# Performance work log

Measured on AMD Instinct MI355X. Metric: run time of the kernel, lower is better.

Reference implementation:

```python
import jax, jax.numpy as jnp
from jax import lax
import numpy as np

NUM_LAYERS, HIDDEN, INPUT, OUT = 6, 256, 128, 10
B, T = 128, 512


def setup_inputs() -> dict:
    key = jax.random.key(0)
    ks = jax.random.split(key, 9)
    s = 0.05  # keep gate pre-activations in a sane range
    return {
        "x": jax.random.normal(ks[0], (B, T, INPUT), jnp.float32),
        "h0": jax.random.normal(ks[1], (NUM_LAYERS, B, HIDDEN), jnp.float32) * s,
        "c0": jax.random.normal(ks[2], (NUM_LAYERS, B, HIDDEN), jnp.float32) * s,
        "w_ih": jax.random.normal(ks[3], (NUM_LAYERS, 4 * HIDDEN, HIDDEN), jnp.float32) * s,
        "w_hh": jax.random.normal(ks[4], (NUM_LAYERS, 4 * HIDDEN, HIDDEN), jnp.float32) * s,
        "b_ih": jax.random.normal(ks[5], (NUM_LAYERS, 4 * HIDDEN), jnp.float32) * s,
        "b_hh": jax.random.normal(ks[6], (NUM_LAYERS, 4 * HIDDEN), jnp.float32) * s,
        "fc_w": jax.random.normal(ks[7], (OUT, HIDDEN), jnp.float32) * s,
        "fc_b": jax.random.normal(ks[8], (OUT,), jnp.float32) * s,
    }


def _lstm_layer(xseq, h, c, wih, whh, bih, bhh):
    # xseq: [B,T,D]; precompute input-to-gate GEMM for the whole sequence.
    gx = jnp.einsum("btd,gd->btg", xseq, wih) + (bih + bhh)  # [B,T,4H]

    def step(carry, g_t):
        h, c = carry
        g = g_t + h @ whh.T  # [B,4H], PyTorch gate order i,f,g,o
        i, f, gg, o = jnp.split(g, 4, axis=-1)
        c = jax.nn.sigmoid(f) * c + jax.nn.sigmoid(i) * jnp.tanh(gg)
        h = jax.nn.sigmoid(o) * jnp.tanh(c)
        return (h, c), h

    (_, _), hs = lax.scan(step, (h, c), jnp.swapaxes(gx, 0, 1))  # hs: [T,B,H]
    return jnp.swapaxes(hs, 0, 1)  # [B,T,H]


def reference(x, h0, c0, w_ih, w_hh, b_ih, b_hh, fc_w, fc_b):
    # Zero-pad input features 128 -> 256 so the packed [4H,256] layer-0 w_ih
    # applies identically to using its first 128 columns.
    seq = jnp.pad(x, ((0, 0), (0, 0), (0, HIDDEN - INPUT)))
    for l in range(NUM_LAYERS):
        seq = _lstm_layer(seq, h0[l], c0[l], w_ih[l], w_hh[l], b_ih[l], b_hh[l])
    return seq[:, -1, :] @ fc_w.T + fc_b  # [B,OUT]
```

## Files before the change

### kernel.cpp

```cpp
#include <hip/hip_runtime.h>
#include <stdint.h>

#define NLAYER 6
#define BATCH  128
#define HID    256
#define TSEQ   512
#define INFEAT 128
#define DEPTH  8
#define OUTN   10

typedef __attribute__((ext_vector_type(8))) short bf16x8;
typedef __attribute__((ext_vector_type(4))) float f32x4;

__device__ __forceinline__ short f2bf(float f) {
  union { float f; uint32_t u; } v; v.f = f;
  uint32_t r = v.u + 0x7fffu + ((v.u >> 16) & 1u);
  return (short)(r >> 16);
}
__device__ __forceinline__ float bf2f(uint32_t b) {
  union { uint32_t u; float f; } v; v.u = b << 16;
  return v.f;
}
__device__ __forceinline__ bf16x8 cvt8(const float* p) {
  f32x4 a = *(const f32x4*)p;
  f32x4 b = *(const f32x4*)(p + 4);
  bf16x8 r;
  r[0] = f2bf(a[0]); r[1] = f2bf(a[1]); r[2] = f2bf(a[2]); r[3] = f2bf(a[3]);
  r[4] = f2bf(b[0]); r[5] = f2bf(b[1]); r[6] = f2bf(b[2]); r[7] = f2bf(b[3]);
  return r;
}
__device__ __forceinline__ float sigm(float x)  { return 1.0f / (1.0f + __expf(-x)); }
__device__ __forceinline__ float tanhff(float x){ return 1.0f - 2.0f / (__expf(2.0f * x) + 1.0f); }

__device__ __forceinline__ bf16x8 load_frag_dc(const uint16_t* p) {
  union { unsigned long long q[2]; bf16x8 v; } u;
  u.q[0] = __hip_atomic_load((const unsigned long long*)p,
                             __ATOMIC_RELAXED, __HIP_MEMORY_SCOPE_AGENT);
  u.q[1] = __hip_atomic_load((const unsigned long long*)(p + 4),
                             __ATOMIC_RELAXED, __HIP_MEMORY_SCOPE_AGENT);
  return u.v;
}
__device__ __forceinline__ void store_u16_dc(uint16_t* p, uint16_t v) {
  __hip_atomic_store(p, v, __ATOMIC_RELAXED, __HIP_MEMORY_SCOPE_AGENT);
}
__device__ __forceinline__ void store_u8_dc(uint8_t* p, uint8_t v) {
  __hip_atomic_store(p, v, __ATOMIC_RELAXED, __HIP_MEMORY_SCOPE_AGENT);
}
__device__ __forceinline__ bool rec_half(const uint8_t* f) {
  unsigned long long a = __hip_atomic_load((const unsigned long long*)f,
                                           __ATOMIC_RELAXED, __HIP_MEMORY_SCOPE_AGENT);
  unsigned long long b = __hip_atomic_load((const unsigned long long*)(f + 8),
                                           __ATOMIC_RELAXED, __HIP_MEMORY_SCOPE_AGENT);
  return ((a & b) == 0x0101010101010101ULL);
}

__global__ void __launch_bounds__(256, 1)
lstm_pipeline(const float* __restrict__ xin, const float* __restrict__ h0,
              const float* __restrict__ c0,  const float* __restrict__ wih,
              const float* __restrict__ whh, const float* __restrict__ bih,
              const float* __restrict__ bhh, const float* __restrict__ fcw,
              const float* __restrict__ fcb, float* __restrict__ out,
              uint8_t* flags, uint16_t* hbuf)
{
  const int bid  = blockIdx.x;
  const int xcd  = bid & 7;
  const int slot = bid >> 3;
  const int grp  = (slot >> 3) * 8 + xcd;
  const int cg   = slot & 7;
  const int l  = grp >> 2;
  const int bs = grp & 3;

  const int tid  = threadIdx.x;
  const int wv   = tid >> 6, lane = tid & 63;
  const int wm   = wv & 1,  wu   = wv >> 1;
  const int l15  = lane & 15, l4 = lane >> 4;

  __shared__ bf16x8 lds_wih[4096];
  {
    const float* W = wih + (size_t)l * 1024 * 256;
    for (int lin = tid; lin < 4096; lin += 256) {
      const int l4s = lin & 3;
      const int u5  = (lin >> 2) & 31;
      const int kk  = (lin >> 7) & 7;
      const int gt  = lin >> 10;
      const int row = gt * 256 + cg * 32 + u5;
      lds_wih[lin] = cvt8(W + (size_t)row * 256 + kk * 32 + l4s * 8);
    }
  }

  bf16x8 wh[4][8];
  float  bias[4];
  {
    const float* W = whh + (size_t)l * 1024 * 256;
#pragma unroll
    for (int gt = 0; gt < 4; ++gt) {
      const int Rg = gt * 256 + cg * 32 + wu * 16 + l15;
      const float* rp = W + (size_t)Rg * 256 + l4 * 8;
#pragma unroll
      for (int kk = 0; kk < 8; ++kk)
        wh[gt][kk] = cvt8(rp + kk * 32);
      bias[gt] = bih[l * 1024 + Rg] + bhh[l * 1024 + Rg];
    }
  }
  __syncthreads();

  const int ucol  = cg * 32 + wu * 16 + l15;
  const int mrowA = bs * 32 + wm * 16 + l15;
  const int mrow0 = bs * 32 + wm * 16 + l4*4;

  float c[4];
#pragma unroll
  for (int j = 0; j < 4; ++j)
    c[j] = c0[((size_t)l * BATCH + (mrow0 + j)) * HID + ucol];

  const uint8_t* fXr = (l > 0) ? flags + ((size_t)((l - 1) * 4 + bs) * TSEQ) * 32 : nullptr;
  uint8_t*       fOr = flags + ((size_t)grp * TSEQ) * 32;
  const uint8_t* fCr = (l < 5) ? flags + ((size_t)((l + 1) * 4 + bs) * TSEQ) * 32 : nullptr;

  const uint16_t* hbL = hbuf + (size_t)l * DEPTH * BATCH * HID;
  const uint16_t* hbX = (l > 0) ? hbuf + (size_t)(l - 1) * DEPTH * BATCH * HID : nullptr;
  uint16_t*       hbO = hbuf + (size_t)l * DEPTH * BATCH * HID;

  const int fidx = wm * 16 + cg * 2 + wu;

  for (int t = 0; t < TSEQ; ++t) {
    {
      bool needx = (l > 0), needh = (t > 0);
      const uint8_t* fx = needx ? fXr + (size_t)t * 32 + wm * 16 : nullptr;
      const uint8_t* fo = needh ? fOr + (size_t)(t - 1) * 32 + wm * 16 : nullptr;
      while (needx || needh) {
        if (needx && rec_half(fx)) needx = false;
        if (needh && rec_half(fo)) needh = false;
      }
    }

    bf16x8 ah[8];
    if (t == 0) {
      const float* hp = h0 + ((size_t)l * BATCH + mrowA) * HID + l4 * 8;
#pragma unroll
      for (int kk = 0; kk < 8; ++kk) ah[kk] = cvt8(hp + kk * 32);
    } else {
      const uint16_t* hp = hbL + ((size_t)((t - 1) & (DEPTH - 1)) * BATCH + mrowA) * HID + l4 * 8;
#pragma unroll
      for (int kk = 0; kk < 8; ++kk) ah[kk] = load_frag_dc(hp + kk * 32);
    }

    f32x4 acc[4];
#pragma unroll
    for (int gt = 0; gt < 4; ++gt) {
      f32x4 a = {bias[gt], bias[gt], bias[gt], bias[gt]};
      acc[gt] = a;
    }

    const int bbase = (wu * 16 + l15) * 4 + l4;
    if (l == 0) {
      const float* xp = xin + ((size_t)mrowA * TSEQ + t) * INFEAT + l4 * 8;
#pragma unroll
      for (int kk = 0; kk < 4; ++kk) {
        bf16x8 axr = cvt8(xp + kk * 32);
#pragma unroll
        for (int gt = 0; gt < 4; ++gt) {
          bf16x8 b = lds_wih[gt * 1024 + kk * 128 + bbase];
          acc[gt] = __builtin_amdgcn_mfma_f32_16x16x32_bf16(axr, b, acc[gt], 0, 0, 0);
        }
      }
    } else {
      bf16x8 ax[8];
      const uint16_t* hp = hbX + ((size_t)(t & (DEPTH - 1)) * BATCH + mrowA) * HID + l4 * 8;
#pragma unroll
      for (int kk = 0; kk < 8; ++kk) ax[kk] = load_frag_dc(hp + kk * 32);
#pragma unroll
      for (int kk = 0; kk < 8; ++kk) {
#pragma unroll
        for (int gt = 0; gt < 4; ++gt) {
          bf16x8 b = lds_wih[gt * 1024 + kk * 128 + bbase];
          acc[gt] = __builtin_amdgcn_mfma_f32_16x16x32_bf16(ax[kk], b, acc[gt], 0, 0, 0);
        }
      }
    }

#pragma unroll
    for (int kk = 0; kk < 8; ++kk)
#pragma unroll
      for (int gt = 0; gt < 4; ++gt)
        acc[gt] = __builtin_amdgcn_mfma_f32_16x16x32_bf16(ah[kk], wh[gt][kk], acc[gt], 0, 0, 0);

    if (l < 5 && t >= DEPTH) {
      const uint8_t* fc = fCr + (size_t)(t - DEPTH) * 32 + wm * 16;
      while (!rec_half(fc)) __builtin_amdgcn_s_sleep(2);
    }

    uint16_t* op = hbO + (size_t)(t & (DEPTH - 1)) * BATCH * HID;
#pragma unroll
    for (int j = 0; j < 4; ++j) {
      float iv = sigm(acc[0][j]);
      float fv = sigm(acc[1][j]);
      float gv = tanhff(acc[2][j]);
      float ov = sigm(acc[3][j]);
      float cc = fv * c[j] + iv * gv;
      c[j] = cc;
      float hv = ov * tanhff(cc);
      store_u16_dc(op + (size_t)(mrow0 + j) * HID + ucol, (uint16_t)f2bf(hv));
    }
    asm volatile("s_waitcnt vmcnt(0)" ::: "memory");
    if (lane == 0)
      store_u8_dc(fOr + (size_t)t * 32 + fidx, (uint8_t)1);
  }

  if (l == 5 && cg == 0) {
    const uint8_t* fl = fOr + (size_t)(TSEQ - 1) * 32;
    while (!(rec_half(fl) && rec_half(fl + 16))) __builtin_amdgcn_s_sleep(1);
    const uint16_t* hp = hbL + (size_t)((TSEQ - 1) & (DEPTH - 1)) * BATCH * HID;
    for (int p = tid; p < 32 * OUTN; p += 256) {
      const int mr = bs * 32 + p / OUTN, oc = p % OUTN;
      float a = fcb[oc];
      const uint16_t* hr = hp + (size_t)mr * HID;
      const float* wr = fcw + oc * HID;
#pragma unroll
      for (int uu = 0; uu < HID; uu += 4) {
        unsigned long long q = __hip_atomic_load((const unsigned long long*)(hr + uu),
                                                 __ATOMIC_RELAXED, __HIP_MEMORY_SCOPE_AGENT);
        a += bf2f((uint32_t)(q & 0xffff))         * wr[uu]
           + bf2f((uint32_t)((q >> 16) & 0xffff)) * wr[uu + 1]
           + bf2f((uint32_t)((q >> 32) & 0xffff)) * wr[uu + 2]
           + bf2f((uint32_t)(q >> 48))            * wr[uu + 3];
      }
      out[mr * OUTN + oc] = a;
    }
  }
}

extern "C" void kernel_launch(void* const* d_in, const int* in_sizes, int n_in,
                              void* d_out, int out_size, void* d_ws, size_t ws_size,
                              hipStream_t stream) {
  const float* xin = (const float*)d_in[0];
  const float* h0  = (const float*)d_in[1];
  const float* c0  = (const float*)d_in[2];
  const float* wih = (const float*)d_in[3];
  const float* whh = (const float*)d_in[4];
  const float* bih = (const float*)d_in[5];
  const float* bhh = (const float*)d_in[6];
  const float* fcw = (const float*)d_in[7];
  const float* fcb = (const float*)d_in[8];
  float* out = (float*)d_out;

  uint8_t* flags = (uint8_t*)d_ws;
  const size_t flagBytes = (size_t)24 * TSEQ * 32;
  uint16_t* hbuf = (uint16_t*)((char*)d_ws + 0x80000);

  hipMemsetAsync(d_ws, 0, flagBytes, stream);
  lstm_pipeline<<<dim3(192), dim3(256), 0, stream>>>(
      xin, h0, c0, wih, whh, bih, bhh, fcw, fcb, out, flags, hbuf);
}
```

Measured before the change: 3.419 ms.

## Replace per-step flag handshakes with tagged data words and progress counters

Each hidden-state store now packs two bf16 values with a 16-bit timestep tag into one 64-bit word. Consumers spin directly on the data until every tag matches, which removes the separate flag store and the vmcnt(0) drain that sat on the recurrent critical path. Back-pressure now uses per-wave progress counters instead of per-timestep flag arrays, the ring shrinks to depth 4, and the LDS weight layout is reordered. In exchange, ring traffic doubles because of the tag bits, and correctness relies on stale tags from earlier runs never matching, since the ring is no longer cleared.

```diff
diff --git a/kernel.cpp b/kernel.cpp
--- a/kernel.cpp
+++ b/kernel.cpp
@@ -6,11 +6,12 @@
 #define HID    256
 #define TSEQ   512
 #define INFEAT 128
-#define DEPTH  8
+#define DEPTH  4
 #define OUTN   10
 
 typedef __attribute__((ext_vector_type(8))) short bf16x8;
 typedef __attribute__((ext_vector_type(4))) float f32x4;
+typedef unsigned long long u64;
 
 __device__ __forceinline__ short f2bf(float f) {
   union { float f; uint32_t u; } v; v.f = f;
@@ -32,27 +33,16 @@
 __device__ __forceinline__ float sigm(float x)  { return 1.0f / (1.0f + __expf(-x)); }
 __device__ __forceinline__ float tanhff(float x){ return 1.0f - 2.0f / (__expf(2.0f * x) + 1.0f); }
 
-__device__ __forceinline__ bf16x8 load_frag_dc(const uint16_t* p) {
-  union { unsigned long long q[2]; bf16x8 v; } u;
-  u.q[0] = __hip_atomic_load((const unsigned long long*)p,
-                             __ATOMIC_RELAXED, __HIP_MEMORY_SCOPE_AGENT);
-  u.q[1] = __hip_atomic_load((const unsigned long long*)(p + 4),
-                             __ATOMIC_RELAXED, __HIP_MEMORY_SCOPE_AGENT);
-  return u.v;
-}
-__device__ __forceinline__ void store_u16_dc(uint16_t* p, uint16_t v) {
+__device__ __forceinline__ u64 ld64(const u64* p) {
+  return __hip_atomic_load(p, __ATOMIC_RELAXED, __HIP_MEMORY_SCOPE_AGENT);
+}
+__device__ __forceinline__ void st64(u64* p, u64 v) {
   __hip_atomic_store(p, v, __ATOMIC_RELAXED, __HIP_MEMORY_SCOPE_AGENT);
 }
-__device__ __forceinline__ void store_u8_dc(uint8_t* p, uint8_t v) {
+__device__ __forceinline__ void st16(uint16_t* p, uint16_t v) {
   __hip_atomic_store(p, v, __ATOMIC_RELAXED, __HIP_MEMORY_SCOPE_AGENT);
 }
-__device__ __forceinline__ bool rec_half(const uint8_t* f) {
-  unsigned long long a = __hip_atomic_load((const unsigned long long*)f,
-                                           __ATOMIC_RELAXED, __HIP_MEMORY_SCOPE_AGENT);
-  unsigned long long b = __hip_atomic_load((const unsigned long long*)(f + 8),
-                                           __ATOMIC_RELAXED, __HIP_MEMORY_SCOPE_AGENT);
-  return ((a & b) == 0x0101010101010101ULL);
-}
+
 
 __global__ void __launch_bounds__(256, 1)
 lstm_pipeline(const float* __restrict__ xin, const float* __restrict__ h0,
@@ -60,7 +50,7 @@
               const float* __restrict__ whh, const float* __restrict__ bih,
               const float* __restrict__ bhh, const float* __restrict__ fcw,
               const float* __restrict__ fcb, float* __restrict__ out,
-              uint8_t* flags, uint16_t* hbuf)
+              uint16_t* prog, u64* ring)
 {
   const int bid  = blockIdx.x;
   const int xcd  = bid & 7;
@@ -79,8 +69,8 @@
   {
     const float* W = wih + (size_t)l * 1024 * 256;
     for (int lin = tid; lin < 4096; lin += 256) {
-      const int l4s = lin & 3;
-      const int u5  = (lin >> 2) & 31;
+      const int u5  = lin & 31;
+      const int l4s = (lin >> 5) & 3;
       const int kk  = (lin >> 7) & 7;
       const int gt  = lin >> 10;
       const int row = gt * 256 + cg * 32 + u5;
@@ -106,43 +96,47 @@
 
   const int ucol  = cg * 32 + wu * 16 + l15;
   const int mrowA = bs * 32 + wm * 16 + l15;
-  const int mrow0 = bs * 32 + wm * 16 + l4*4;
+  const int mrow0 = bs * 32 + wm * 16 + l4 * 4;
 
   float c[4];
 #pragma unroll
   for (int j = 0; j < 4; ++j)
     c[j] = c0[((size_t)l * BATCH + (mrow0 + j)) * HID + ucol];
 
-  const uint8_t* fXr = (l > 0) ? flags + ((size_t)((l - 1) * 4 + bs) * TSEQ) * 32 : nullptr;
-  uint8_t*       fOr = flags + ((size_t)grp * TSEQ) * 32;
-  const uint8_t* fCr = (l < 5) ? flags + ((size_t)((l + 1) * 4 + bs) * TSEQ) * 32 : nullptr;
-
-  const uint16_t* hbL = hbuf + (size_t)l * DEPTH * BATCH * HID;
-  const uint16_t* hbX = (l > 0) ? hbuf + (size_t)(l - 1) * DEPTH * BATCH * HID : nullptr;
-  uint16_t*       hbO = hbuf + (size_t)l * DEPTH * BATCH * HID;
-
-  const int fidx = wm * 16 + cg * 2 + wu;
+  u64*       ringO = ring + (size_t)l * DEPTH * BATCH * 128;
+  const u64* ringL = ringO;
+  const u64* ringX = (l > 0) ? ring + (size_t)(l - 1) * DEPTH * BATCH * 128 : nullptr;
+
+  uint16_t* progOwn = prog + (l * 4 + bs) * 32;
+  const u64* progCons = (l < 5) ? (const u64*)(prog + ((l + 1) * 4 + bs) * 32) : nullptr;
+
+  const int srow = bs * 32 + wm * 16 + 15;
 
   for (int t = 0; t < TSEQ; ++t) {
+    if (lane == 0)
+      st16(progOwn + (cg * 4 + wv), (uint16_t)t);
+
     {
-      bool needx = (l > 0), needh = (t > 0);
-      const uint8_t* fx = needx ? fXr + (size_t)t * 32 + wm * 16 : nullptr;
-      const uint8_t* fo = needh ? fOr + (size_t)(t - 1) * 32 + wm * 16 : nullptr;
-      while (needx || needh) {
-        if (needx && rec_half(fx)) needx = false;
-        if (needh && rec_half(fo)) needh = false;
-      }
-    }
-
-    bf16x8 ah[8];
-    if (t == 0) {
-      const float* hp = h0 + ((size_t)l * BATCH + mrowA) * HID + l4 * 8;
-#pragma unroll
-      for (int kk = 0; kk < 8; ++kk) ah[kk] = cvt8(hp + kk * 32);
-    } else {
-      const uint16_t* hp = hbL + ((size_t)((t - 1) & (DEPTH - 1)) * BATCH + mrowA) * HID + l4 * 8;
-#pragma unroll
-      for (int kk = 0; kk < 8; ++kk) ah[kk] = load_frag_dc(hp + kk * 32);
+      const bool isH = (lane < 16), isX = (lane >= 16 && lane < 32);
+      const bool needS = (isH && t > 0) || (isX && l > 0);
+      const u64* sp = ringL;
+      u64 stag = 0;
+      if (isH && t > 0) {
+        const int cgp = lane >> 1, wup = lane & 1;
+        sp = ringL + (((size_t)((t - 1) & (DEPTH - 1)) * BATCH + srow) * 128 + cgp * 16 + wup * 8 + 7);
+        stag = (u64)t;
+      } else if (isX && l > 0) {
+        const int i = lane - 16, cgp = i >> 1, wup = i & 1;
+        sp = ringX + (((size_t)(t & (DEPTH - 1)) * BATCH + srow) * 128 + cgp * 16 + wup * 8 + 7);
+        stag = (u64)(t + 1);
+      }
+      if (t > 0 || l > 0) {
+        for (;;) {
+          int ok = 1;
+          if (needS) ok = ((ld64(sp) >> 48) == stag);
+          if (__all(ok)) break;
+        }
+      }
     }
 
     f32x4 acc[4];
@@ -152,45 +146,97 @@
       acc[gt] = a;
     }
 
-    const int bbase = (wu * 16 + l15) * 4 + l4;
+    const int bcol = wu * 16 + l15;
     if (l == 0) {
       const float* xp = xin + ((size_t)mrowA * TSEQ + t) * INFEAT + l4 * 8;
 #pragma unroll
       for (int kk = 0; kk < 4; ++kk) {
         bf16x8 axr = cvt8(xp + kk * 32);
 #pragma unroll
-        for (int gt = 0; gt < 4; ++gt) {
-          bf16x8 b = lds_wih[gt * 1024 + kk * 128 + bbase];
-          acc[gt] = __builtin_amdgcn_mfma_f32_16x16x32_bf16(axr, b, acc[gt], 0, 0, 0);
+        for (int gt = 0; gt < 4; ++gt)
+          acc[gt] = __builtin_amdgcn_mfma_f32_16x16x32_bf16(
+              axr, lds_wih[((gt * 8 + kk) * 4 + l4) * 32 + bcol], acc[gt], 0, 0, 0);
+      }
+    } else {
+      const u64* xb = ringX + ((size_t)(t & (DEPTH - 1)) * BATCH + mrowA) * 128 + l4 * 4;
+      const u64 tagX = (u64)(t + 1);
+      bf16x8 ax[8];
+      for (;;) {
+        u64 bad = 0;
+#pragma unroll
+        for (int kk = 0; kk < 8; ++kk) {
+          union { uint32_t w[4]; bf16x8 v; } u;
+#pragma unroll
+          for (int j = 0; j < 4; ++j) {
+            u64 r = ld64(xb + kk * 16 + j);
+            bad |= (r >> 48) ^ tagX;
+            u.w[j] = (uint32_t)r;
+          }
+          ax[kk] = u.v;
         }
+        if (__all(bad == 0)) break;
+      }
+#pragma unroll
+      for (int kk = 0; kk < 8; ++kk)
+#pragma unroll
+        for (int gt = 0; gt < 4; ++gt)
+          acc[gt] = __builtin_amdgcn_mfma_f32_16x16x32_bf16(
+              ax[kk], lds_wih[((gt * 8 + kk) * 4 + l4) * 32 + bcol], acc[gt], 0, 0, 0);
+    }
+
+    if (t == 0) {
+      const float* hp = h0 + ((size_t)l * BATCH + mrowA) * HID + l4 * 8;
+#pragma unroll
+      for (int kk = 0; kk < 8; ++kk) {
+        bf16x8 af = cvt8(hp + kk * 32);
+#pragma unroll
+        for (int gt = 0; gt < 4; ++gt)
+          acc[gt] = __builtin_amdgcn_mfma_f32_16x16x32_bf16(af, wh[gt][kk], acc[gt], 0, 0, 0);
       }
     } else {
-      bf16x8 ax[8];
-      const uint16_t* hp = hbX + ((size_t)(t & (DEPTH - 1)) * BATCH + mrowA) * HID + l4 * 8;
-#pragma unroll
-      for (int kk = 0; kk < 8; ++kk) ax[kk] = load_frag_dc(hp + kk * 32);
-#pragma unroll
-      for (int kk = 0; kk < 8; ++kk) {
-#pragma unroll
-        for (int gt = 0; gt < 4; ++gt) {
-          bf16x8 b = lds_wih[gt * 1024 + kk * 128 + bbase];
-          acc[gt] = __builtin_amdgcn_mfma_f32_16x16x32_bf16(ax[kk], b, acc[gt], 0, 0, 0);
+      const u64* hb = ringL + ((size_t)((t - 1) & (DEPTH - 1)) * BATCH + mrowA) * 128 + l4 * 4;
+      const u64 tagH = (u64)t;
+      bf16x8 ah[8];
+      for (;;) {
+        u64 bad = 0;
+#pragma unroll
+        for (int kk = 0; kk < 8; ++kk) {
+          union { uint32_t w[4]; bf16x8 v; } u;
+#pragma unroll
+          for (int j = 0; j < 4; ++j) {
+            u64 r = ld64(hb + kk * 16 + j);
+            bad |= (r >> 48) ^ tagH;
+            u.w[j] = (uint32_t)r;
+          }
+          ah[kk] = u.v;
         }
-      }
-    }
-
-#pragma unroll
-    for (int kk = 0; kk < 8; ++kk)
-#pragma unroll
-      for (int gt = 0; gt < 4; ++gt)
-        acc[gt] = __builtin_amdgcn_mfma_f32_16x16x32_bf16(ah[kk], wh[gt][kk], acc[gt], 0, 0, 0);
+        if (__all(bad == 0)) break;
+      }
+#pragma unroll
+      for (int kk = 0; kk < 8; ++kk)
+#pragma unroll
+        for (int gt = 0; gt < 4; ++gt)
+          acc[gt] = __builtin_amdgcn_mfma_f32_16x16x32_bf16(ah[kk], wh[gt][kk], acc[gt], 0, 0, 0);
+    }
 
     if (l < 5 && t >= DEPTH) {
-      const uint8_t* fc = fCr + (size_t)(t - DEPTH) * 32 + wm * 16;
-      while (!rec_half(fc)) __builtin_amdgcn_s_sleep(2);
-    }
-
-    uint16_t* op = hbO + (size_t)(t & (DEPTH - 1)) * BATCH * HID;
+      const int need = t - (DEPTH - 1);
+      for (;;) {
+        int mn = 0x7fffffff;
+#pragma unroll
+        for (int q = 0; q < 8; ++q) {
+          u64 v = ld64(progCons + q);
+          mn = min(mn, (int)(v & 0xffff));
+          mn = min(mn, (int)((v >> 16) & 0xffff));
+          mn = min(mn, (int)((v >> 32) & 0xffff));
+          mn = min(mn, (int)((v >> 48) & 0xffff));
+        }
+        if (mn >= need) break;
+        __builtin_amdgcn_s_sleep(2);
+      }
+    }
+
+    uint32_t hv16[4];
 #pragma unroll
     for (int j = 0; j < 4; ++j) {
       float iv = sigm(acc[0][j]);
@@ -200,30 +246,43 @@
       float cc = fv * c[j] + iv * gv;
       c[j] = cc;
       float hv = ov * tanhff(cc);
-      store_u16_dc(op + (size_t)(mrow0 + j) * HID + ucol, (uint16_t)f2bf(hv));
-    }
-    asm volatile("s_waitcnt vmcnt(0)" ::: "memory");
-    if (lane == 0)
-      store_u8_dc(fOr + (size_t)t * 32 + fidx, (uint8_t)1);
+      hv16[j] = (uint32_t)(uint16_t)f2bf(hv);
+    }
+    {
+      const uint32_t own01 = hv16[0] | (hv16[1] << 16);
+      const uint32_t own23 = hv16[2] | (hv16[3] << 16);
+      const uint32_t par01 = (uint32_t)__shfl_xor((int)own01, 1);
+      const uint32_t par23 = (uint32_t)__shfl_xor((int)own23, 1);
+      const u64 tagS = (u64)(t + 1) << 48;
+      uint32_t d0, d1; int j0;
+      if ((l15 & 1) == 0) {
+        d0 = (own01 & 0xffffu) | (par01 << 16);
+        d1 = (own01 >> 16)     | (par01 & 0xffff0000u);
+        j0 = 0;
+      } else {
+        d0 = (par23 & 0xffffu) | (own23 << 16);
+        d1 = (par23 >> 16)     | (own23 & 0xffff0000u);
+        j0 = 2;
+      }
+      u64* rp = ringO + ((size_t)(t & (DEPTH - 1)) * BATCH + (mrow0 + j0)) * 128 + (ucol >> 1);
+      st64(rp,       (u64)d0 | tagS);
+      st64(rp + 128, (u64)d1 | tagS);
+    }
   }
 
   if (l == 5 && cg == 0) {
-    const uint8_t* fl = fOr + (size_t)(TSEQ - 1) * 32;
-    while (!(rec_half(fl) && rec_half(fl + 16))) __builtin_amdgcn_s_sleep(1);
-    const uint16_t* hp = hbL + (size_t)((TSEQ - 1) & (DEPTH - 1)) * BATCH * HID;
+    const u64* hsl = ring + (size_t)5 * DEPTH * BATCH * 128
+                   + ((size_t)((TSEQ - 1) & (DEPTH - 1)) * BATCH) * 128;
     for (int p = tid; p < 32 * OUTN; p += 256) {
       const int mr = bs * 32 + p / OUTN, oc = p % OUTN;
       float a = fcb[oc];
-      const uint16_t* hr = hp + (size_t)mr * HID;
+      const u64* hr = hsl + (size_t)mr * 128;
       const float* wr = fcw + oc * HID;
-#pragma unroll
-      for (int uu = 0; uu < HID; uu += 4) {
-        unsigned long long q = __hip_atomic_load((const unsigned long long*)(hr + uu),
-                                                 __ATOMIC_RELAXED, __HIP_MEMORY_SCOPE_AGENT);
-        a += bf2f((uint32_t)(q & 0xffff))         * wr[uu]
-           + bf2f((uint32_t)((q >> 16) & 0xffff)) * wr[uu + 1]
-           + bf2f((uint32_t)((q >> 32) & 0xffff)) * wr[uu + 2]
-           + bf2f((uint32_t)(q >> 48))            * wr[uu + 3];
+      for (int up = 0; up < 128; ++up) {
+        u64 r = ld64(hr + up);
+        while ((r >> 48) != (u64)TSEQ) r = ld64(hr + up);
+        a += bf2f((uint32_t)(r & 0xffff))         * wr[2 * up]
+           + bf2f((uint32_t)((r >> 16) & 0xffff)) * wr[2 * up + 1];
       }
       out[mr * OUTN + oc] = a;
     }
@@ -244,11 +303,10 @@
   const float* fcb = (const float*)d_in[8];
   float* out = (float*)d_out;
 
-  uint8_t* flags = (uint8_t*)d_ws;
-  const size_t flagBytes = (size_t)24 * TSEQ * 32;
-  uint16_t* hbuf = (uint16_t*)((char*)d_ws + 0x80000);
-
-  hipMemsetAsync(d_ws, 0, flagBytes, stream);
+  uint16_t* prog = (uint16_t*)d_ws;
+  u64* ring = (u64*)((char*)d_ws + 0x10000);
+
+  hipMemsetAsync(d_ws, 0, 4096, stream);
   lstm_pipeline<<<dim3(192), dim3(256), 0, stream>>>(
-      xin, h0, c0, wih, whh, bih, bhh, fcw, fcb, out, flags, hbuf);
-}
+      xin, h0, c0, wih, whh, bih, bhh, fcw, fcb, out, prog, ring);
+}
```

After: 5.229 ms. 1.53x slower.
